# Optimization experiments

Hardware: AMD Instinct MI355X
Metric: run time of the kernel (lower is better)

## Reference

```python
import jax, jax.numpy as jnp
import numpy as np

N_NODES = 50000
N_EDGES = 800000
D_IN = 128
D_OUT = 128


def setup_inputs() -> dict:
    key = jax.random.key(0)
    k1, k2, k3, k4, k5 = jax.random.split(key, 5)
    gain = float(np.sqrt(2.0))  # calculate_gain('relu')
    # xavier_uniform bound: gain * sqrt(6/(fan_in+fan_out))
    bound = gain * float(np.sqrt(6.0 / (D_IN + D_OUT)))
    feat = jax.random.normal(k1, (N_NODES, D_IN), dtype=jnp.float32)
    weight = jax.random.uniform(k2, (D_IN, D_OUT), minval=-bound, maxval=bound, dtype=jnp.float32)
    loop_weight = jax.random.uniform(k3, (D_IN, D_OUT), minval=-bound, maxval=bound, dtype=jnp.float32)
    h_bias = jnp.zeros((D_OUT,), dtype=jnp.float32)
    src = jax.random.randint(k4, (N_EDGES,), 0, N_NODES, dtype=jnp.int32)
    dst = jax.random.randint(k5, (N_EDGES,), 0, N_NODES, dtype=jnp.int32)
    return {"feat": feat, "weight": weight, "h_bias": h_bias,
            "loop_weight": loop_weight, "src": src, "dst": dst}


def reference(feat, weight, h_bias, loop_weight, src, dst):
    # message: m_e = feat[src_e] @ W ; aggregate: h_v = sum_{e: dst_e=v} m_e
    # (equivalently transform-then-gather, which avoids the [E, D] matmul)
    transformed = feat @ weight                    # [N, D_out]
    msgs = transformed[src]                        # [E, D_out] gather
    h = jax.ops.segment_sum(msgs, dst, num_segments=feat.shape[0])  # [N, D_out]
    h = h + h_bias                                 # bias
    h = h + feat @ loop_weight                     # self-loop
    # activation=None, dropout=0 -> identity
    return h
```

## Files before the change

### kernel.cpp

```cpp
#include <hip/hip_runtime.h>

#define D 128
#define CAP 64
#define FCHUNK 4096
#define LROW 264

typedef __attribute__((ext_vector_type(8))) short bf16x8;
typedef __attribute__((ext_vector_type(4))) float f32x4;

__device__ inline unsigned short f2bf_rne(float x) {
    unsigned u = __float_as_uint(x);
    return (unsigned short)((u + 0x7FFFu + ((u >> 16) & 1u)) >> 16);
}
__device__ inline float bf_lo(unsigned u) { return __uint_as_float(u << 16); }
__device__ inline float bf_hi(unsigned u) { return __uint_as_float(u & 0xFFFF0000u); }

__global__ __launch_bounds__(256) void prep_kernel(
    const float* __restrict__ W, const float* __restrict__ LW,
    unsigned short* __restrict__ Bt, int* __restrict__ cursor, int ncur)
{
    int tid = blockIdx.x * 256 + threadIdx.x;
    if (tid < 2 * D * D) {
        int n = tid >> 7;
        int k = tid & 127;
        float v = (n < D) ? W[(size_t)k * D + n] : LW[(size_t)k * D + (n - D)];
        Bt[(size_t)n * D + k] = f2bf_rne(v);
    }
    int j = tid - 2 * D * D;
    if (j >= 0 && j < ncur) cursor[j] = 0;
}

__global__ __launch_bounds__(256) void fill_kernel(
    const int* __restrict__ src, const int* __restrict__ dst,
    int* __restrict__ cursor, unsigned short* __restrict__ ebuf,
    int E, int cstride)
{
    const int chunk = blockIdx.x >> 3;
    const int cls   = blockIdx.x & 7;
    const int base  = chunk * FCHUNK;

    for (int i = threadIdx.x; i < FCHUNK; i += 256) {
        const int e = base + i;
        if (e >= E) break;
        const int d = dst[e];
        const int s = src[e];
        if ((d & 7) == cls) {
            int pos = atomicAdd(&cursor[(cls * cstride) + (d >> 3)], 1);
            if (pos < CAP) ebuf[(size_t)d * CAP + pos] = (unsigned short)s;
        }
    }
}

__global__ __launch_bounds__(256) void mfma_transform(
    const float* __restrict__ feat, const unsigned short* __restrict__ Bt,
    unsigned short* __restrict__ T2, int N)
{
    __shared__ unsigned short tile[4 * 16 * LROW];
    const int wave = threadIdx.x >> 6;
    const int lane = threadIdx.x & 63;
    const int wrow0 = blockIdx.x * 64 + wave * 16;
    const int m    = lane & 15;
    const int kg   = lane >> 4;

    int arow_idx = wrow0 + m;
    if (arow_idx >= N) arow_idx = N - 1;
    const float* arow = feat + (size_t)arow_idx * D;

    bf16x8 a[4];
#pragma unroll
    for (int ks = 0; ks < 4; ++ks) {
        const float4 f0 = *(const float4*)(arow + ks * 32 + kg * 8);
        const float4 f1 = *(const float4*)(arow + ks * 32 + kg * 8 + 4);
        bf16x8 v;
        v[0] = (short)f2bf_rne(f0.x); v[1] = (short)f2bf_rne(f0.y);
        v[2] = (short)f2bf_rne(f0.z); v[3] = (short)f2bf_rne(f0.w);
        v[4] = (short)f2bf_rne(f1.x); v[5] = (short)f2bf_rne(f1.y);
        v[6] = (short)f2bf_rne(f1.z); v[7] = (short)f2bf_rne(f1.w);
        a[ks] = v;
    }

    f32x4 acc[16];
#pragma unroll
    for (int t = 0; t < 16; ++t) acc[t] = (f32x4){0.f, 0.f, 0.f, 0.f};

#pragma unroll
    for (int t = 0; t < 16; ++t) {
        const unsigned short* brow = Bt + (size_t)(t * 16 + m) * D;
        bf16x8 b0 = *(const bf16x8*)(brow + 0 * 32 + kg * 8);
        bf16x8 b1 = *(const bf16x8*)(brow + 1 * 32 + kg * 8);
        bf16x8 b2 = *(const bf16x8*)(brow + 2 * 32 + kg * 8);
        bf16x8 b3 = *(const bf16x8*)(brow + 3 * 32 + kg * 8);
        acc[t] = __builtin_amdgcn_mfma_f32_16x16x32_bf16(a[0], b0, acc[t], 0, 0, 0);
        acc[t] = __builtin_amdgcn_mfma_f32_16x16x32_bf16(a[1], b1, acc[t], 0, 0, 0);
        acc[t] = __builtin_amdgcn_mfma_f32_16x16x32_bf16(a[2], b2, acc[t], 0, 0, 0);
        acc[t] = __builtin_amdgcn_mfma_f32_16x16x32_bf16(a[3], b3, acc[t], 0, 0, 0);
    }

    unsigned short* wtile = tile + wave * 16 * LROW;
#pragma unroll
    for (int t = 0; t < 16; ++t) {
#pragma unroll
        for (int r = 0; r < 4; ++r)
            wtile[(kg * 4 + r) * LROW + t * 16 + m] = f2bf_rne(acc[t][r]);
    }
    __syncthreads();

#pragma unroll
    for (int i = 0; i < 8; ++i) {
        const int f   = i * 64 + lane;
        const int row = f >> 5;
        const int cs  = f & 31;
        if (wrow0 + row < N) {
            const uint4 v = *(const uint4*)(wtile + row * LROW + cs * 8);
            *(uint4*)(T2 + (size_t)(wrow0 + row) * 256 + cs * 8) = v;
        }
    }
}

__global__ __launch_bounds__(256) void gather_kernel(
    const unsigned short* __restrict__ ebuf, const int* __restrict__ cursor,
    const unsigned short* __restrict__ T2, const float* __restrict__ bias,
    float* __restrict__ out, int N, int cstride)
{
    const int node = (blockIdx.x * 256 + threadIdx.x) >> 6;
    const int lane = threadIdx.x & 63;
    if (node >= N) return;

    const int h = lane >> 5;
    const int q = lane & 31;

    int deg = cursor[((node & 7) * cstride) + (node >> 3)];
    if (deg > CAP) deg = CAP;

    const unsigned* region = (const unsigned*)(ebuf + (size_t)node * CAP);
    const unsigned short* Tq = T2 + q * 4;

    float a0 = 0.f, a1 = 0.f, a2 = 0.f, a3 = 0.f;

    for (int j = 0; j < deg; j += 16) {
        uint2 u[8];
#pragma unroll
        for (int k = 0; k < 8; ++k) {
            const unsigned w = region[(j >> 1) + k];
            const unsigned s = h ? (w >> 16) : (w & 0xFFFFu);
            u[k] = *(const uint2*)(Tq + (size_t)s * 256);
        }
#pragma unroll
        for (int k = 0; k < 8; ++k) {
            const bool live = (j + 2 * k + h) < deg;
            a0 += live ? bf_lo(u[k].x) : 0.f;
            a1 += live ? bf_hi(u[k].x) : 0.f;
            a2 += live ? bf_lo(u[k].y) : 0.f;
            a3 += live ? bf_hi(u[k].y) : 0.f;
        }
    }

    a0 += __shfl_xor(a0, 32, 64);
    a1 += __shfl_xor(a1, 32, 64);
    a2 += __shfl_xor(a2, 32, 64);
    a3 += __shfl_xor(a3, 32, 64);

    if (h == 0) {
        const uint2 sv = *(const uint2*)(T2 + (size_t)node * 256 + 128 + q * 4);
        const float4 b = *(const float4*)(bias + q * 4);
        float4 o;
        o.x = b.x + bf_lo(sv.x) + a0;
        o.y = b.y + bf_hi(sv.x) + a1;
        o.z = b.z + bf_lo(sv.y) + a2;
        o.w = b.w + bf_hi(sv.y) + a3;
        *(float4*)(out + (size_t)node * D + q * 4) = o;
    }
}

extern "C" void kernel_launch(void* const* d_in, const int* in_sizes, int n_in,
                              void* d_out, int out_size, void* d_ws, size_t ws_size,
                              hipStream_t stream) {
    const float* feat = (const float*)d_in[0];
    const float* W    = (const float*)d_in[1];
    const float* bias = (const float*)d_in[2];
    const float* LW   = (const float*)d_in[3];
    const int*   src  = (const int*)d_in[4];
    const int*   dst  = (const int*)d_in[5];
    float* out = (float*)d_out;

    const int N = in_sizes[0] / D;
    const int E = in_sizes[4];
    const int cstride = (N + 7) >> 3;
    const int ncur = 8 * cstride;

    unsigned short* T2   = (unsigned short*)d_ws;
    unsigned short* Bt   = T2 + (size_t)N * 256;
    unsigned short* ebuf = Bt + 2 * D * D;
    int* cursor = (int*)(ebuf + (size_t)N * CAP);

    {
        const int work = 2 * D * D + ncur;
        prep_kernel<<<dim3((work + 255) / 256), 256, 0, stream>>>(W, LW, Bt, cursor, ncur);
    }

    {
        const int nchunks = (E + FCHUNK - 1) / FCHUNK;
        fill_kernel<<<dim3(nchunks * 8), 256, 0, stream>>>(src, dst, cursor, ebuf, E, cstride);
    }

    mfma_transform<<<dim3((N + 63) / 64), 256, 0, stream>>>(feat, Bt, T2, N);

    gather_kernel<<<dim3((N + 3) / 4), 256, 0, stream>>>(ebuf, cursor, T2, bias, out, N, cstride);
}
```

Measured before the change: 189.9 us.

## Unroll edge fill, reorder gather nodes by class, mask dead gathers, nontemporal stores

Several independent tweaks land together. The fill kernel now uses a smaller chunk with a fully unrolled loop and predicated loads. The gather kernel maps nodes so that blocks follow the cursor class layout, redirects out-of-range neighbor indices to row 0, and writes output with nontemporal stores. The __syncthreads in the transform kernel is removed, which is safe only because each wave reads back only its own tile region. The gather remap produces strided node writes, and the dead-lane redirection replaces a garbage read with a read of row 0.

```diff
diff --git a/kernel.cpp b/kernel.cpp
--- a/kernel.cpp
+++ b/kernel.cpp
@@ -2,7 +2,7 @@
 
 #define D 128
 #define CAP 64
-#define FCHUNK 4096
+#define FCHUNK 2048
 #define LROW 264
 
 typedef __attribute__((ext_vector_type(8))) short bf16x8;
@@ -37,15 +37,16 @@
 {
     const int chunk = blockIdx.x >> 3;
     const int cls   = blockIdx.x & 7;
-    const int base  = chunk * FCHUNK;
-
-    for (int i = threadIdx.x; i < FCHUNK; i += 256) {
-        const int e = base + i;
-        if (e >= E) break;
-        const int d = dst[e];
-        const int s = src[e];
-        if ((d & 7) == cls) {
-            int pos = atomicAdd(&cursor[(cls * cstride) + (d >> 3)], 1);
+    const int base  = chunk * FCHUNK + threadIdx.x;
+
+#pragma unroll
+    for (int ii = 0; ii < FCHUNK / 256; ++ii) {
+        const int e  = base + ii * 256;
+        const bool ok = (e < E);
+        const int d = ok ? dst[e] : -1;
+        const int s = ok ? src[e] : 0;
+        if (ok && (d & 7) == cls) {
+            const int pos = atomicAdd(&cursor[(cls * cstride) + (d >> 3)], 1);
             if (pos < CAP) ebuf[(size_t)d * CAP + pos] = (unsigned short)s;
         }
     }
@@ -103,7 +104,6 @@
         for (int r = 0; r < 4; ++r)
             wtile[(kg * 4 + r) * LROW + t * 16 + m] = f2bf_rne(acc[t][r]);
     }
-    __syncthreads();
 
 #pragma unroll
     for (int i = 0; i < 8; ++i) {
@@ -122,14 +122,16 @@
     const unsigned short* __restrict__ T2, const float* __restrict__ bias,
     float* __restrict__ out, int N, int cstride)
 {
-    const int node = (blockIdx.x * 256 + threadIdx.x) >> 6;
+    const int cls  = blockIdx.x & 7;
+    const int w    = threadIdx.x >> 6;
+    const int node = (((int)(blockIdx.x >> 3) * 4 + w) * 8) + cls;
     const int lane = threadIdx.x & 63;
     if (node >= N) return;
 
     const int h = lane >> 5;
     const int q = lane & 31;
 
-    int deg = cursor[((node & 7) * cstride) + (node >> 3)];
+    int deg = cursor[(cls * cstride) + (node >> 3)];
     if (deg > CAP) deg = CAP;
 
     const unsigned* region = (const unsigned*)(ebuf + (size_t)node * CAP);
@@ -141,8 +143,9 @@
         uint2 u[8];
 #pragma unroll
         for (int k = 0; k < 8; ++k) {
-            const unsigned w = region[(j >> 1) + k];
-            const unsigned s = h ? (w >> 16) : (w & 0xFFFFu);
+            const unsigned w32 = region[(j >> 1) + k];
+            unsigned s = h ? (w32 >> 16) : (w32 & 0xFFFFu);
+            if (j + 2 * k + h >= deg) s = 0;
             u[k] = *(const uint2*)(Tq + (size_t)s * 256);
         }
 #pragma unroll
@@ -163,12 +166,12 @@
     if (h == 0) {
         const uint2 sv = *(const uint2*)(T2 + (size_t)node * 256 + 128 + q * 4);
         const float4 b = *(const float4*)(bias + q * 4);
-        float4 o;
+        f32x4 o;
         o.x = b.x + bf_lo(sv.x) + a0;
         o.y = b.y + bf_hi(sv.x) + a1;
         o.z = b.z + bf_lo(sv.y) + a2;
         o.w = b.w + bf_hi(sv.y) + a3;
-        *(float4*)(out + (size_t)node * D + q * 4) = o;
+        __builtin_nontemporal_store(o, (f32x4*)(out + (size_t)node * D + q * 4));
     }
 }
 
@@ -205,5 +208,9 @@
 
     mfma_transform<<<dim3((N + 63) / 64), 256, 0, stream>>>(feat, Bt, T2, N);
 
-    gather_kernel<<<dim3((N + 3) / 4), 256, 0, stream>>>(ebuf, cursor, T2, bias, out, N, cstride);
-}
+    {
+        const int bpc = (cstride + 3) / 4;
+        gather_kernel<<<dim3(8 * bpc), 256, 0, stream>>>(
+            ebuf, cursor, T2, bias, out, N, cstride);
+    }
+}
```

After: 187.6 us. No clear change (-1.2%).
